# Optimization experiments

Measured on AMD Instinct MI355X. Metric: run time of the kernel, lower is better.

Reference implementation:

```python
import jax, jax.numpy as jnp
import numpy as np

EPS = 1e-12  # torch F.normalize eps


def setup_inputs() -> dict:
    key = jax.random.key(0)
    k1, k2, k3 = jax.random.split(key, 3)
    b, c, h, w = 4, 192, 128, 128
    num_heads = 8
    in1 = jax.random.normal(k1, (b, c, h, w), dtype=jnp.float32)
    in2 = jax.random.normal(k2, (b, c, h, w), dtype=jnp.float32)
    scale = jnp.ones((num_heads, 1, 1), dtype=jnp.float32)
    proj_w = jax.random.normal(k3, (c, c), dtype=jnp.float32) * (1.0 / np.sqrt(c))
    return {"in1": in1, "in2": in2, "scale": scale, "proj_w": proj_w, "num_heads": num_heads}


def reference(in1, in2, scale, proj_w, num_heads):
    b, c, h, w = in1.shape
    hd = c // num_heads
    hw = h * w
    # b (head c) h w -> b head c (h w)
    q = in1.reshape(b, num_heads, hd, hw)
    k = in2.reshape(b, num_heads, hd, hw)
    # L2-normalize along the (h w) axis, torch eps semantics
    q = q / jnp.maximum(jnp.linalg.norm(q, axis=-1, keepdims=True), EPS)
    k = k / jnp.maximum(jnp.linalg.norm(k, axis=-1, keepdims=True), EPS)
    # channel-wise attention: [b, head, c, c]
    attn = jnp.einsum('bhcn,bhdn->bhcd', q, k) * scale  # scale broadcasts [head,1,1]
    attn = jax.nn.softmax(attn, axis=-1)
    out = jnp.einsum('bhcd,bhdn->bhcn', attn, k)
    out = out.reshape(b, c, h, w)
    # 1x1 conv projection (no bias)
    out = jnp.einsum('oc,bchw->bohw', proj_w, out)
    return out
```

## Files before the change

### kernel.cpp

```cpp
#include <hip/hip_runtime.h>
#include <hip/hip_bf16.h>
#include <math.h>

#define BATCH 4
#define NHEAD 8
#define HD 24
#define CH 192
#define HW 16384
#define SPL 32
#define SROW 640

#define OFF_MO  (32 * SPL * SROW)
#define OFF_CNT (OFF_MO + (BATCH * CH * CH) / 2)
#define OFF_KBF 729600

#define LSTR 132

typedef __attribute__((ext_vector_type(8)))  short bf16x8;
typedef __attribute__((ext_vector_type(16))) float f32x16;

__device__ __forceinline__ unsigned short bf16rne(float x) {
    union { float f; unsigned u; } v; v.f = x;
    unsigned u = v.u;
    return (unsigned short)((u + 0x7FFFu + ((u >> 16) & 1u)) >> 16);
}

__device__ __forceinline__ unsigned pack2(float a, float b) {
    union { __hip_bfloat162 h; unsigned u; } c;
    c.h = __float22bfloat162_rn(float2{a, b});
    return c.u;
}

__device__ __forceinline__ void st_agent(float* p, float v) {
    __hip_atomic_store(p, v, __ATOMIC_RELAXED, __HIP_MEMORY_SCOPE_AGENT);
}
__device__ __forceinline__ float ld_agent(const float* p) {
    return __hip_atomic_load(p, __ATOMIC_RELAXED, __HIP_MEMORY_SCOPE_AGENT);
}

__global__ __launch_bounds__(256, 4) void kA(const float* __restrict__ q,
                                             const float* __restrict__ k,
                                             const float* __restrict__ scale,
                                             const float* __restrict__ w,
                                             float* __restrict__ ws,
                                             unsigned short* __restrict__ Mo,
                                             unsigned int* __restrict__ cnt,
                                             unsigned int* __restrict__ kbf) {
    __shared__ unsigned int tile[2][HD * LSTR];
    __shared__ int lastFlag;

    const int bh   = blockIdx.x;
    const int cb   = blockIdx.y;
    const int t    = threadIdx.x;
    const int lane = t & 63;
    const int wave = t >> 6;
    const int m    = lane & 31;
    const int hi   = lane >> 5;
    const int rowc = (m < HD) ? m : 0;

    f32x16 aQK = {}, aQQ = {}, aKK = {};

    #pragma unroll
    for (int half = 0; half < 2; ++half) {
        const float* qb = q + (size_t)bh * HD * HW + cb * 512 + half * 256;
        const float* kb = k + (size_t)bh * HD * HW + cb * 512 + half * 256;

        #pragma unroll
        for (int j = 0; j < 6; ++j) {
            const int idx = j * 256 + t;
            const int row = idx >> 6;
            const int c64 = idx & 63;
            float4 qv = *(const float4*)(qb + (size_t)row * HW + c64 * 4);
            float4 kv = *(const float4*)(kb + (size_t)row * HW + c64 * 4);
            uint2 qp = make_uint2(pack2(qv.x, qv.y), pack2(qv.z, qv.w));
            uint2 kp = make_uint2(pack2(kv.x, kv.y), pack2(kv.z, kv.w));
            *(uint2*)&tile[0][row * LSTR + c64 * 2] = qp;
            *(uint2*)&tile[1][row * LSTR + c64 * 2] = kp;
            kbf[(((size_t)(bh * HD + row)) << 13) + (cb << 8) + half * 128 + (c64 << 1)]     = kp.x;
            kbf[(((size_t)(bh * HD + row)) << 13) + (cb << 8) + half * 128 + (c64 << 1) + 1] = kp.y;
        }
        __syncthreads();

        #pragma unroll
        for (int s = 0; s < 4; ++s) {
            const int off = (wave * 64 + s * 16) >> 1;
            bf16x8 aq = *(const bf16x8*)&tile[0][rowc * LSTR + off + hi * 4];
            bf16x8 bk = *(const bf16x8*)&tile[1][rowc * LSTR + off + hi * 4];
            aQK = __builtin_amdgcn_mfma_f32_32x32x16_bf16(aq, bk, aQK, 0, 0, 0);
            aQQ = __builtin_amdgcn_mfma_f32_32x32x16_bf16(aq, aq, aQQ, 0, 0, 0);
            aKK = __builtin_amdgcn_mfma_f32_32x32x16_bf16(bk, bk, aKK, 0, 0, 0);
        }
        __syncthreads();
    }

    float* red = (float*)tile;
    if (m < HD) {
        #pragma unroll
        for (int r = 0; r < 16; ++r) {
            const int i = (r & 3) + 8 * (r >> 2) + 4 * hi;
            if (i < HD) {
                red[wave * 624 + i * HD + m] = aQK[r];
                if (i == m) {
                    red[wave * 624 + 576 + i] = aQQ[r];
                    red[wave * 624 + 600 + i] = aKK[r];
                }
            }
        }
    }
    __syncthreads();

    float* Srow = ws + ((size_t)bh * SPL + cb) * SROW;
    for (int e = t; e < 624; e += 256)
        st_agent(&Srow[e], red[e] + red[624 + e] + red[1248 + e] + red[1872 + e]);

    asm volatile("s_waitcnt vmcnt(0)" ::: "memory");
    __syncthreads();

    if (t == 0) {
        unsigned int old = __hip_atomic_fetch_add(&cnt[bh], 1u,
                                                  __ATOMIC_RELAXED,
                                                  __HIP_MEMORY_SCOPE_AGENT);
        lastFlag = (old == SPL - 1);
    }
    __syncthreads();
    if (!lastFlag) return;

    float* sf = (float*)tile;
    const int b = bh >> 3;
    const int h = bh & 7;
    const float* base = ws + (size_t)bh * SPL * SROW;

    for (int idx = t; idx < CH * HD; idx += 256) {
        int o = idx / HD, dd = idx - o * HD;
        sf[672 + idx] = w[o * CH + h * HD + dd];
    }
    for (int e = t; e < 624; e += 256) {
        float s0 = 0.f, s1 = 0.f, s2 = 0.f, s3 = 0.f;
        #pragma unroll
        for (int sp = 0; sp < SPL; sp += 4) {
            s0 += ld_agent(&base[(size_t)(sp + 0) * SROW + e]);
            s1 += ld_agent(&base[(size_t)(sp + 1) * SROW + e]);
            s2 += ld_agent(&base[(size_t)(sp + 2) * SROW + e]);
            s3 += ld_agent(&base[(size_t)(sp + 3) * SROW + e]);
        }
        sf[e] = (s0 + s1) + (s2 + s3);
    }
    __syncthreads();

    if (t < 2 * HD) {
        float inv = 1.0f / fmaxf(sqrtf(sf[576 + t]), 1e-12f);
        sf[624 + t] = inv;
    }
    __syncthreads();

    const float sc = scale[h];
    for (int e = t; e < 576; e += 256)
        sf[e] = sf[e] * sf[624 + e / HD] * sf[648 + e % HD] * sc;
    __syncthreads();

    if (t < HD) {
        float mx = -1e30f;
        for (int j = 0; j < HD; ++j) mx = fmaxf(mx, sf[t * HD + j]);
        float sum = 0.f;
        for (int j = 0; j < HD; ++j) {
            float v = expf(sf[t * HD + j] - mx);
            sf[t * HD + j] = v;
            sum += v;
        }
        float r = 1.0f / sum;
        for (int j = 0; j < HD; ++j) sf[t * HD + j] *= r;
    }
    __syncthreads();

    for (int idx = t; idx < CH * HD; idx += 256) {
        int o = idx / HD, j = idx - o * HD;
        float v = 0.f;
        #pragma unroll
        for (int i = 0; i < HD; ++i)
            v = fmaf(sf[672 + o * HD + i], sf[i * HD + j], v);
        Mo[(size_t)b * CH * CH + (size_t)o * CH + h * HD + j] = bf16rne(v * sf[648 + j]);
    }
}

#define KCN 64
#define BSTR3 100

__global__ __launch_bounds__(256, 4) void kC(const unsigned int* __restrict__ kbf,
                                             const unsigned short* __restrict__ Mo,
                                             float* __restrict__ out) {
    __shared__ unsigned int Bt[KCN * BSTR3];

    const int t    = threadIdx.x;
    const int lane = t & 63;
    const int wave = t >> 6;
    const int n31  = lane & 31;
    const int hi   = lane >> 5;
    const int nt   = wave & 1;
    const int otb  = (wave >> 1) * 3;

    const int nb = blockIdx.x * KCN;
    const int b  = blockIdx.y;

    const unsigned short* Mob = Mo + (size_t)b * CH * CH;

    unsigned short* bt16 = (unsigned short*)Bt;
    #pragma unroll
    for (int i = 0; i < 6; ++i) {
        const int idx = i * 256 + t;
        const int ch  = idx >> 3;
        const int sl  = idx & 7;
        uint4 v4 = *(const uint4*)(kbf + (((size_t)(b * CH + ch)) << 13) +
                                   ((size_t)blockIdx.x << 5) + (sl << 2));
        #pragma unroll
        for (int jj = 0; jj < 8; ++jj)
            bt16[(sl * 8 + jj) * (BSTR3 * 2) + ch] = ((const unsigned short*)&v4)[jj];
    }
    __syncthreads();

    f32x16 acc[3] = {};
    #pragma unroll
    for (int kc = 0; kc < 12; ++kc) {
        bf16x8 Bf = *(const bf16x8*)&Bt[(nt * 32 + n31) * BSTR3 + kc * 8 + hi * 4];
        #pragma unroll
        for (int oi = 0; oi < 3; ++oi) {
            const unsigned short* ap =
                Mob + (size_t)((otb + oi) * 32 + n31) * CH + kc * 16 + hi * 8;
            bf16x8 Af = *(const bf16x8*)ap;
            acc[oi] = __builtin_amdgcn_mfma_f32_32x32x16_bf16(Af, Bf, acc[oi], 0, 0, 0);
        }
    }

    float* op = out + (size_t)b * CH * HW;
    const int n = nb + nt * 32 + n31;
    #pragma unroll
    for (int oi = 0; oi < 3; ++oi)
        #pragma unroll
        for (int r = 0; r < 16; ++r) {
            int o = (otb + oi) * 32 + (r & 3) + 8 * (r >> 2) + 4 * hi;
            op[(size_t)o * HW + n] = acc[oi][r];
        }
}

extern "C" void kernel_launch(void* const* d_in, const int* in_sizes, int n_in,
                              void* d_out, int out_size, void* d_ws, size_t ws_size,
                              hipStream_t stream) {
    const float* in1   = (const float*)d_in[0];
    const float* in2   = (const float*)d_in[1];
    const float* scale = (const float*)d_in[2];
    const float* projw = (const float*)d_in[3];
    float* ws  = (float*)d_ws;
    float* out = (float*)d_out;
    unsigned short* Mo = (unsigned short*)(ws + OFF_MO);
    unsigned int* cnt  = (unsigned int*)(ws + OFF_CNT);
    unsigned int* kbf  = (unsigned int*)(ws + OFF_KBF);

    hipMemsetAsync((void*)cnt, 0, 32 * sizeof(unsigned int), stream);
    kA<<<dim3(32, SPL), 256, 0, stream>>>(in1, in2, scale, projw, ws, Mo, cnt, kbf);
    kC<<<dim3(HW / KCN, BATCH), 256, 0, stream>>>(kbf, Mo, out);
}
```

Baseline: 176.1 us.

## Fuse Gram and projection kernels into one persistent launch with spin-wait flags

Merges the two kernels into a single 1024-block launch. Each block first does its Gram-partial work, then acts as an output-GEMM block that spins on per-column-chunk and per-batch counters before reading the bf16 K copy and the folded Mo matrix. This removes the kernel-boundary drain and one launch. The Mo epilogue also now packs two bf16 values per store. The risk is spin deadlock if not all blocks are co-resident: 1024 blocks at 4 per CU fits on 256 CUs, but there is no guarantee. Polling also costs some time.

```diff
diff --git a/kernel.cpp b/kernel.cpp
--- a/kernel.cpp
+++ b/kernel.cpp
@@ -15,15 +15,11 @@
 #define OFF_KBF 729600
 
 #define LSTR 132
+#define KCN 64
+#define BSTR3 100
 
 typedef __attribute__((ext_vector_type(8)))  short bf16x8;
 typedef __attribute__((ext_vector_type(16))) float f32x16;
-
-__device__ __forceinline__ unsigned short bf16rne(float x) {
-    union { float f; unsigned u; } v; v.f = x;
-    unsigned u = v.u;
-    return (unsigned short)((u + 0x7FFFu + ((u >> 16) & 1u)) >> 16);
-}
 
 __device__ __forceinline__ unsigned pack2(float a, float b) {
     union { __hip_bfloat162 h; unsigned u; } c;
@@ -34,23 +30,33 @@
 __device__ __forceinline__ void st_agent(float* p, float v) {
     __hip_atomic_store(p, v, __ATOMIC_RELAXED, __HIP_MEMORY_SCOPE_AGENT);
 }
+__device__ __forceinline__ void st_agent_u(unsigned int* p, unsigned int v) {
+    __hip_atomic_store(p, v, __ATOMIC_RELAXED, __HIP_MEMORY_SCOPE_AGENT);
+}
 __device__ __forceinline__ float ld_agent(const float* p) {
     return __hip_atomic_load(p, __ATOMIC_RELAXED, __HIP_MEMORY_SCOPE_AGENT);
 }
-
-__global__ __launch_bounds__(256, 4) void kA(const float* __restrict__ q,
-                                             const float* __restrict__ k,
-                                             const float* __restrict__ scale,
-                                             const float* __restrict__ w,
-                                             float* __restrict__ ws,
-                                             unsigned short* __restrict__ Mo,
-                                             unsigned int* __restrict__ cnt,
-                                             unsigned int* __restrict__ kbf) {
-    __shared__ unsigned int tile[2][HD * LSTR];
+__device__ __forceinline__ unsigned int ld_agent_u(const unsigned int* p) {
+    return __hip_atomic_load(p, __ATOMIC_RELAXED, __HIP_MEMORY_SCOPE_AGENT);
+}
+
+__global__ __launch_bounds__(256, 4) void fused(const float* __restrict__ q,
+                                                const float* __restrict__ k,
+                                                const float* __restrict__ scale,
+                                                const float* __restrict__ w,
+                                                float* __restrict__ ws,
+                                                unsigned short* __restrict__ Mo,
+                                                unsigned int* __restrict__ sem,
+                                                unsigned int* __restrict__ kbf,
+                                                float* __restrict__ out) {
+    __shared__ unsigned int arena[KCN * BSTR3];
     __shared__ int lastFlag;
 
-    const int bh   = blockIdx.x;
-    const int cb   = blockIdx.y;
+    unsigned int* cnt  = sem;
+    unsigned int* kcnt = sem + 32;
+    unsigned int* fin  = sem + 64;
+
+    const int bid  = blockIdx.x;
     const int t    = threadIdx.x;
     const int lane = t & 63;
     const int wave = t >> 6;
@@ -58,169 +64,190 @@
     const int hi   = lane >> 5;
     const int rowc = (m < HD) ? m : 0;
 
-    f32x16 aQK = {}, aQQ = {}, aKK = {};
-
-    #pragma unroll
-    for (int half = 0; half < 2; ++half) {
-        const float* qb = q + (size_t)bh * HD * HW + cb * 512 + half * 256;
-        const float* kb = k + (size_t)bh * HD * HW + cb * 512 + half * 256;
-
-        #pragma unroll
-        for (int j = 0; j < 6; ++j) {
-            const int idx = j * 256 + t;
-            const int row = idx >> 6;
-            const int c64 = idx & 63;
-            float4 qv = *(const float4*)(qb + (size_t)row * HW + c64 * 4);
-            float4 kv = *(const float4*)(kb + (size_t)row * HW + c64 * 4);
-            uint2 qp = make_uint2(pack2(qv.x, qv.y), pack2(qv.z, qv.w));
-            uint2 kp = make_uint2(pack2(kv.x, kv.y), pack2(kv.z, kv.w));
-            *(uint2*)&tile[0][row * LSTR + c64 * 2] = qp;
-            *(uint2*)&tile[1][row * LSTR + c64 * 2] = kp;
-            kbf[(((size_t)(bh * HD + row)) << 13) + (cb << 8) + half * 128 + (c64 << 1)]     = kp.x;
-            kbf[(((size_t)(bh * HD + row)) << 13) + (cb << 8) + half * 128 + (c64 << 1) + 1] = kp.y;
-        }
-        __syncthreads();
-
-        #pragma unroll
-        for (int s = 0; s < 4; ++s) {
-            const int off = (wave * 64 + s * 16) >> 1;
-            bf16x8 aq = *(const bf16x8*)&tile[0][rowc * LSTR + off + hi * 4];
-            bf16x8 bk = *(const bf16x8*)&tile[1][rowc * LSTR + off + hi * 4];
-            aQK = __builtin_amdgcn_mfma_f32_32x32x16_bf16(aq, bk, aQK, 0, 0, 0);
-            aQQ = __builtin_amdgcn_mfma_f32_32x32x16_bf16(aq, aq, aQQ, 0, 0, 0);
-            aKK = __builtin_amdgcn_mfma_f32_32x32x16_bf16(bk, bk, aKK, 0, 0, 0);
-        }
-        __syncthreads();
-    }
-
-    float* red = (float*)tile;
-    if (m < HD) {
-        #pragma unroll
-        for (int r = 0; r < 16; ++r) {
-            const int i = (r & 3) + 8 * (r >> 2) + 4 * hi;
-            if (i < HD) {
-                red[wave * 624 + i * HD + m] = aQK[r];
-                if (i == m) {
-                    red[wave * 624 + 576 + i] = aQQ[r];
-                    red[wave * 624 + 600 + i] = aKK[r];
+    const int bh = bid >> 5;
+    const int cb = bid & 31;
+    {
+        unsigned int (*tile)[HD * LSTR] = (unsigned int (*)[HD * LSTR])arena;
+        f32x16 aQK = {}, aQQ = {}, aKK = {};
+
+        #pragma unroll
+        for (int half = 0; half < 2; ++half) {
+            const float* qb = q + (size_t)bh * HD * HW + cb * 512 + half * 256;
+            const float* kb = k + (size_t)bh * HD * HW + cb * 512 + half * 256;
+
+            #pragma unroll
+            for (int j = 0; j < 6; ++j) {
+                const int idx = j * 256 + t;
+                const int row = idx >> 6;
+                const int c64 = idx & 63;
+                float4 qv = *(const float4*)(qb + (size_t)row * HW + c64 * 4);
+                float4 kv = *(const float4*)(kb + (size_t)row * HW + c64 * 4);
+                uint2 qp = make_uint2(pack2(qv.x, qv.y), pack2(qv.z, qv.w));
+                uint2 kp = make_uint2(pack2(kv.x, kv.y), pack2(kv.z, kv.w));
+                *(uint2*)&tile[0][row * LSTR + c64 * 2] = qp;
+                *(uint2*)&tile[1][row * LSTR + c64 * 2] = kp;
+                const size_t kidx = (((size_t)(bh * HD + row)) << 13) +
+                                    (cb << 8) + half * 128 + (c64 << 1);
+                st_agent_u(&kbf[kidx],     kp.x);
+                st_agent_u(&kbf[kidx + 1], kp.y);
+            }
+            __syncthreads();
+
+            #pragma unroll
+            for (int s = 0; s < 4; ++s) {
+                const int off = (wave * 64 + s * 16) >> 1;
+                bf16x8 aq = *(const bf16x8*)&tile[0][rowc * LSTR + off + hi * 4];
+                bf16x8 bk = *(const bf16x8*)&tile[1][rowc * LSTR + off + hi * 4];
+                aQK = __builtin_amdgcn_mfma_f32_32x32x16_bf16(aq, bk, aQK, 0, 0, 0);
+                aQQ = __builtin_amdgcn_mfma_f32_32x32x16_bf16(aq, aq, aQQ, 0, 0, 0);
+                aKK = __builtin_amdgcn_mfma_f32_32x32x16_bf16(bk, bk, aKK, 0, 0, 0);
+            }
+            __syncthreads();
+        }
+
+        float* red = (float*)arena;
+        if (m < HD) {
+            #pragma unroll
+            for (int r = 0; r < 16; ++r) {
+                const int i = (r & 3) + 8 * (r >> 2) + 4 * hi;
+                if (i < HD) {
+                    red[wave * 624 + i * HD + m] = aQK[r];
+                    if (i == m) {
+                        red[wave * 624 + 576 + i] = aQQ[r];
+                        red[wave * 624 + 600 + i] = aKK[r];
+                    }
                 }
             }
         }
+        __syncthreads();
+
+        float* Srow = ws + ((size_t)bh * SPL + cb) * SROW;
+        for (int e = t; e < 624; e += 256)
+            st_agent(&Srow[e], red[e] + red[624 + e] + red[1248 + e] + red[1872 + e]);
+
+        asm volatile("s_waitcnt vmcnt(0)" ::: "memory");
+        __syncthreads();
+
+        if (t == 0) {
+            unsigned int old = __hip_atomic_fetch_add(&cnt[bh], 1u,
+                                                      __ATOMIC_RELAXED,
+                                                      __HIP_MEMORY_SCOPE_AGENT);
+            lastFlag = (old == SPL - 1);
+            __hip_atomic_fetch_add(&kcnt[cb], 1u, __ATOMIC_RELAXED,
+                                   __HIP_MEMORY_SCOPE_AGENT);
+        }
+        __syncthreads();
+    }
+
+    if (lastFlag) {
+        float* sf = (float*)arena;
+        const int b = bh >> 3;
+        const int h = bh & 7;
+        const float* base = ws + (size_t)bh * SPL * SROW;
+
+        for (int idx = t; idx < CH * HD; idx += 256) {
+            int o = idx / HD, dd = idx - o * HD;
+            sf[672 + idx] = w[o * CH + h * HD + dd];
+        }
+        for (int e = t; e < 624; e += 256) {
+            float s0 = 0.f, s1 = 0.f, s2 = 0.f, s3 = 0.f;
+            #pragma unroll
+            for (int sp = 0; sp < SPL; sp += 4) {
+                s0 += ld_agent(&base[(size_t)(sp + 0) * SROW + e]);
+                s1 += ld_agent(&base[(size_t)(sp + 1) * SROW + e]);
+                s2 += ld_agent(&base[(size_t)(sp + 2) * SROW + e]);
+                s3 += ld_agent(&base[(size_t)(sp + 3) * SROW + e]);
+            }
+            sf[e] = (s0 + s1) + (s2 + s3);
+        }
+        __syncthreads();
+
+        if (t < 2 * HD) {
+            float inv = 1.0f / fmaxf(sqrtf(sf[576 + t]), 1e-12f);
+            sf[624 + t] = inv;
+        }
+        __syncthreads();
+
+        const float sc = scale[h];
+        for (int e = t; e < 576; e += 256)
+            sf[e] = sf[e] * sf[624 + e / HD] * sf[648 + e % HD] * sc;
+        __syncthreads();
+
+        if (t < HD) {
+            float mx = -1e30f;
+            for (int j = 0; j < HD; ++j) mx = fmaxf(mx, sf[t * HD + j]);
+            float sum = 0.f;
+            for (int j = 0; j < HD; ++j) {
+                float v = expf(sf[t * HD + j] - mx);
+                sf[t * HD + j] = v;
+                sum += v;
+            }
+            float r = 1.0f / sum;
+            for (int j = 0; j < HD; ++j) sf[t * HD + j] *= r;
+        }
+        __syncthreads();
+
+        unsigned int* Mo32 = (unsigned int*)Mo;
+        const size_t mobase = ((size_t)b * CH * CH + (size_t)h * HD) >> 1;
+        for (int idx = t; idx < CH * HD / 2; idx += 256) {
+            int o = idx / 12, jp = idx - o * 12;
+            const int j0 = 2 * jp, j1 = 2 * jp + 1;
+            float v0 = 0.f, v1 = 0.f;
+            #pragma unroll
+            for (int i = 0; i < HD; ++i) {
+                const float wv = sf[672 + o * HD + i];
+                v0 = fmaf(wv, sf[i * HD + j0], v0);
+                v1 = fmaf(wv, sf[i * HD + j1], v1);
+            }
+            st_agent_u(&Mo32[mobase + (size_t)o * (CH / 2) + jp],
+                       pack2(v0 * sf[648 + j0], v1 * sf[648 + j1]));
+        }
+        asm volatile("s_waitcnt vmcnt(0)" ::: "memory");
+        __syncthreads();
+        if (t == 0)
+            __hip_atomic_fetch_add(&fin[b], 1u, __ATOMIC_RELAXED,
+                                   __HIP_MEMORY_SCOPE_AGENT);
     }
     __syncthreads();
 
-    float* Srow = ws + ((size_t)bh * SPL + cb) * SROW;
-    for (int e = t; e < 624; e += 256)
-        st_agent(&Srow[e], red[e] + red[624 + e] + red[1248 + e] + red[1872 + e]);
-
-    asm volatile("s_waitcnt vmcnt(0)" ::: "memory");
+    const int bC   = bid >> 8;
+    const int nblk = bid & 255;
+    const int cbC  = nblk >> 3;
+
+    if (t == 0) {
+        while (ld_agent_u(&kcnt[cbC]) < (unsigned)SPL)
+            __builtin_amdgcn_s_sleep(8);
+    }
     __syncthreads();
 
-    if (t == 0) {
-        unsigned int old = __hip_atomic_fetch_add(&cnt[bh], 1u,
-                                                  __ATOMIC_RELAXED,
-                                                  __HIP_MEMORY_SCOPE_AGENT);
-        lastFlag = (old == SPL - 1);
-    }
-    __syncthreads();
-    if (!lastFlag) return;
-
-    float* sf = (float*)tile;
-    const int b = bh >> 3;
-    const int h = bh & 7;
-    const float* base = ws + (size_t)bh * SPL * SROW;
-
-    for (int idx = t; idx < CH * HD; idx += 256) {
-        int o = idx / HD, dd = idx - o * HD;
-        sf[672 + idx] = w[o * CH + h * HD + dd];
-    }
-    for (int e = t; e < 624; e += 256) {
-        float s0 = 0.f, s1 = 0.f, s2 = 0.f, s3 = 0.f;
-        #pragma unroll
-        for (int sp = 0; sp < SPL; sp += 4) {
-            s0 += ld_agent(&base[(size_t)(sp + 0) * SROW + e]);
-            s1 += ld_agent(&base[(size_t)(sp + 1) * SROW + e]);
-            s2 += ld_agent(&base[(size_t)(sp + 2) * SROW + e]);
-            s3 += ld_agent(&base[(size_t)(sp + 3) * SROW + e]);
-        }
-        sf[e] = (s0 + s1) + (s2 + s3);
-    }
-    __syncthreads();
-
-    if (t < 2 * HD) {
-        float inv = 1.0f / fmaxf(sqrtf(sf[576 + t]), 1e-12f);
-        sf[624 + t] = inv;
-    }
-    __syncthreads();
-
-    const float sc = scale[h];
-    for (int e = t; e < 576; e += 256)
-        sf[e] = sf[e] * sf[624 + e / HD] * sf[648 + e % HD] * sc;
-    __syncthreads();
-
-    if (t < HD) {
-        float mx = -1e30f;
-        for (int j = 0; j < HD; ++j) mx = fmaxf(mx, sf[t * HD + j]);
-        float sum = 0.f;
-        for (int j = 0; j < HD; ++j) {
-            float v = expf(sf[t * HD + j] - mx);
-            sf[t * HD + j] = v;
-            sum += v;
-        }
-        float r = 1.0f / sum;
-        for (int j = 0; j < HD; ++j) sf[t * HD + j] *= r;
-    }
-    __syncthreads();
-
-    for (int idx = t; idx < CH * HD; idx += 256) {
-        int o = idx / HD, j = idx - o * HD;
-        float v = 0.f;
-        #pragma unroll
-        for (int i = 0; i < HD; ++i)
-            v = fmaf(sf[672 + o * HD + i], sf[i * HD + j], v);
-        Mo[(size_t)b * CH * CH + (size_t)o * CH + h * HD + j] = bf16rne(v * sf[648 + j]);
-    }
-}
-
-#define KCN 64
-#define BSTR3 100
-
-__global__ __launch_bounds__(256, 4) void kC(const unsigned int* __restrict__ kbf,
-                                             const unsigned short* __restrict__ Mo,
-                                             float* __restrict__ out) {
-    __shared__ unsigned int Bt[KCN * BSTR3];
-
-    const int t    = threadIdx.x;
-    const int lane = t & 63;
-    const int wave = t >> 6;
-    const int n31  = lane & 31;
-    const int hi   = lane >> 5;
-    const int nt   = wave & 1;
-    const int otb  = (wave >> 1) * 3;
-
-    const int nb = blockIdx.x * KCN;
-    const int b  = blockIdx.y;
-
-    const unsigned short* Mob = Mo + (size_t)b * CH * CH;
-
-    unsigned short* bt16 = (unsigned short*)Bt;
+    unsigned short* bt16 = (unsigned short*)arena;
     #pragma unroll
     for (int i = 0; i < 6; ++i) {
         const int idx = i * 256 + t;
         const int ch  = idx >> 3;
         const int sl  = idx & 7;
-        uint4 v4 = *(const uint4*)(kbf + (((size_t)(b * CH + ch)) << 13) +
-                                   ((size_t)blockIdx.x << 5) + (sl << 2));
+        uint4 v4 = *(const uint4*)(kbf + (((size_t)(bC * CH + ch)) << 13) +
+                                   ((size_t)nblk << 5) + (sl << 2));
         #pragma unroll
         for (int jj = 0; jj < 8; ++jj)
             bt16[(sl * 8 + jj) * (BSTR3 * 2) + ch] = ((const unsigned short*)&v4)[jj];
     }
+
+    if (t == 0) {
+        while (ld_agent_u(&fin[bC]) < (unsigned)NHEAD)
+            __builtin_amdgcn_s_sleep(8);
+    }
     __syncthreads();
+
+    const unsigned short* Mob = Mo + (size_t)bC * CH * CH;
+    const int n31 = lane & 31;
+    const int nt  = wave & 1;
+    const int otb = (wave >> 1) * 3;
 
     f32x16 acc[3] = {};
     #pragma unroll
     for (int kc = 0; kc < 12; ++kc) {
-        bf16x8 Bf = *(const bf16x8*)&Bt[(nt * 32 + n31) * BSTR3 + kc * 8 + hi * 4];
+        bf16x8 Bf = *(const bf16x8*)&arena[(nt * 32 + n31) * BSTR3 + kc * 8 + hi * 4];
         #pragma unroll
         for (int oi = 0; oi < 3; ++oi) {
             const unsigned short* ap =
@@ -230,8 +257,8 @@
         }
     }
 
-    float* op = out + (size_t)b * CH * HW;
-    const int n = nb + nt * 32 + n31;
+    float* op = out + (size_t)bC * CH * HW;
+    const int n = nblk * KCN + nt * 32 + n31;
     #pragma unroll
     for (int oi = 0; oi < 3; ++oi)
         #pragma unroll
@@ -251,10 +278,9 @@
     float* ws  = (float*)d_ws;
     float* out = (float*)d_out;
     unsigned short* Mo = (unsigned short*)(ws + OFF_MO);
-    unsigned int* cnt  = (unsigned int*)(ws + OFF_CNT);
+    unsigned int* sem  = (unsigned int*)(ws + OFF_CNT);
     unsigned int* kbf  = (unsigned int*)(ws + OFF_KBF);
 
-    hipMemsetAsync((void*)cnt, 0, 32 * sizeof(unsigned int), stream);
-    kA<<<dim3(32, SPL), 256, 0, stream>>>(in1, in2, scale, projw, ws, Mo, cnt, kbf);
-    kC<<<dim3(HW / KCN, BATCH), 256, 0, stream>>>(kbf, Mo, out);
-}
+    hipMemsetAsync((void*)sem, 0, 68 * sizeof(unsigned int), stream);
+    fused<<<1024, 256, 0, stream>>>(in1, in2, scale, projw, ws, Mo, sem, kbf, out);
+}
```

Result: slower. 218.4 us (+24.0%).
